# Kernel tuning notes

Measured on AMD Instinct MI355X. Metric: run time of the kernel, lower is better.

## Reference

```python
import jax, jax.numpy as jnp
import numpy as np

N_NODES = 50000
N_EDGES = 800000
D = 128
N_LAYERS = 3
BN_EPS = 1e-5


def setup_inputs() -> dict:
    key = jax.random.key(0)
    ks = jax.random.split(key, 12)
    x = jax.random.normal(ks[0], (N_NODES, D), dtype=jnp.float32)
    edge_index = jax.random.randint(ks[1], (2, N_EDGES), 0, N_NODES, dtype=jnp.int64)
    edge_attr = jnp.zeros((N_EDGES,), dtype=jnp.int32)  # unused by BaseGIN
    edge_weight = jax.random.uniform(ks[2], (N_EDGES,), dtype=jnp.float32)
    s = 1.0 / np.sqrt(D)
    W1 = jax.random.uniform(ks[3], (N_LAYERS, D, D), minval=-s, maxval=s, dtype=jnp.float32)
    b1 = jax.random.uniform(ks[4], (N_LAYERS, D), minval=-s, maxval=s, dtype=jnp.float32)
    W2 = jax.random.uniform(ks[5], (N_LAYERS, D, D), minval=-s, maxval=s, dtype=jnp.float32)
    b2 = jax.random.uniform(ks[6], (N_LAYERS, D), minval=-s, maxval=s, dtype=jnp.float32)
    eps = jnp.zeros((N_LAYERS,), dtype=jnp.float32)          # GIN epsilon, init 0
    gamma = jnp.ones((N_LAYERS, D), dtype=jnp.float32)       # BN weight
    beta = jnp.zeros((N_LAYERS, D), dtype=jnp.float32)       # BN bias
    return {"x": x, "edge_index": edge_index, "edge_attr": edge_attr,
            "edge_weight": edge_weight, "W1": W1, "b1": b1, "W2": W2,
            "b2": b2, "eps": eps, "gamma": gamma, "beta": beta}


def reference(x, edge_index, edge_attr, edge_weight, W1, b1, W2, b2, eps, gamma, beta):
    del edge_attr  # deleted in BaseGIN.forward
    src, dst = edge_index[0], edge_index[1]
    ew = edge_weight[:, None]  # [E, 1], matches edge_weight[:, None] in torch
    n = x.shape[0]
    for i in range(N_LAYERS):
        # GINConv: propagate = scatter-add of gathered x[src] * edge_weight
        msg = x[src] * ew                                   # [E, D]
        agg = jax.ops.segment_sum(msg, dst, num_segments=n)  # [N, D]
        h = (1.0 + eps[i]) * x + agg
        # MLP: Linear -> ReLU -> Linear
        h = jnp.maximum(h @ W1[i] + b1[i], 0.0) @ W2[i] + b2[i]
        # BatchNorm1d (training-mode batch statistics, biased variance)
        mu = jnp.mean(h, axis=0)
        var = jnp.mean((h - mu) ** 2, axis=0)
        h = gamma[i] * (h - mu) * jax.lax.rsqrt(var + BN_EPS) + beta[i]
        h = jnp.maximum(h, 0.0)  # ReLU (dropout p=0.0 -> identity)
        x = x + h  # residual
    return x
```

## Files before the change

kernel.cpp:

```cpp
#include <hip/hip_runtime.h>

#define NN 50000
#define NE 800000
#define DD 128
#define D4 32
#define NBUCK 196
#define CAP 5120
#define BIN_EDGES 8192

typedef __attribute__((ext_vector_type(8))) short short8;
typedef __attribute__((ext_vector_type(4))) float f32x4;

__device__ __forceinline__ unsigned short f2bf(float f) {
    unsigned u = __float_as_uint(f);
    unsigned r = u + 0x7FFF + ((u >> 16) & 1);
    return (unsigned short)(r >> 16);
}
__device__ __forceinline__ float bf2f(unsigned short s) {
    return __uint_as_float(((unsigned)s) << 16);
}


__global__ void x2b(const float4* __restrict__ xin, ushort4* __restrict__ xb) {
    int i = blockIdx.x * blockDim.x + threadIdx.x;
    if (i >= NN * D4) return;
    float4 v = xin[i];
    ushort4 o;
    o.x = f2bf(v.x); o.y = f2bf(v.y); o.z = f2bf(v.z); o.w = f2bf(v.w);
    xb[i] = o;
}


__global__ void prep_wt(const float* __restrict__ W1, const float* __restrict__ W2,
                        unsigned short* __restrict__ Wt) {
    int i = blockIdx.x * blockDim.x + threadIdx.x;
    if (i >= 6 * 16384) return;
    int m = i >> 14;
    int r = i & 16383;
    int n = r >> 7;
    int k = r & 127;
    const float* Ws = (m < 3) ? (W1 + m * 16384) : (W2 + (m - 3) * 16384);
    Wt[i] = f2bf(Ws[k * 128 + n]);
}


__global__ void init_bcur(int* __restrict__ bcur) {
    int t = threadIdx.x;
    if (t < NBUCK) bcur[t] = t * CAP;
}

__global__ void __launch_bounds__(256) bin_pass(const int* __restrict__ ei,
                                                const float* __restrict__ ew,
                                                int* __restrict__ bcur,
                                                int2* __restrict__ staging) {
    __shared__ int cnt[256], off[256], cur[256], gb[256];
    __shared__ int2 bin[BIN_EDGES];
    int tid = threadIdx.x;
    int e0 = blockIdx.x * BIN_EDGES;
    int ne = NE - e0; if (ne > BIN_EDGES) ne = BIN_EDGES;
    cnt[tid] = 0;
    __syncthreads();
    for (int i = tid; i < ne; i += 256) {
        int dst = ei[NE + e0 + i];
        atomicAdd(&cnt[dst >> 8], 1);
    }
    __syncthreads();
    off[tid] = cnt[tid];
    __syncthreads();
    for (int o = 1; o < 256; o <<= 1) {
        int v = off[tid];
        int add = (tid >= o) ? off[tid - o] : 0;
        __syncthreads();
        off[tid] = v + add;
        __syncthreads();
    }
    cur[tid] = off[tid] - cnt[tid];
    __syncthreads();
    for (int i = tid; i < ne; i += 256) {
        int e = e0 + i;
        int dst = ei[NE + e];
        unsigned pack = (((unsigned)ei[e]) << 16) | (unsigned)f2bf(ew[e]);
        int p = atomicAdd(&cur[dst >> 8], 1);
        bin[p] = make_int2((int)pack, dst & 255);
    }
    __syncthreads();
    if (tid < NBUCK) gb[tid] = atomicAdd(&bcur[tid], cnt[tid]);
    __syncthreads();
    for (int i = tid; i < ne; i += 256) {
        int lo = 0, hi = NBUCK - 1;
        while (lo < hi) {
            int mid = (lo + hi) >> 1;
            if (off[mid] > i) hi = mid; else lo = mid + 1;
        }
        int local = i - (off[lo] - cnt[lo]);
        staging[gb[lo] + local] = bin[i];
    }
}

__global__ void scan_buckets(const int* __restrict__ bcur, int* __restrict__ bb2) {
    __shared__ int sh[256];
    int tid = threadIdx.x;
    int c = (tid < NBUCK) ? (bcur[tid] - tid * CAP) : 0;
    sh[tid] = c;
    __syncthreads();
    for (int o = 1; o < 256; o <<= 1) {
        int v = sh[tid];
        int add = (tid >= o) ? sh[tid - o] : 0;
        __syncthreads();
        sh[tid] += 0;
        sh[tid] = v + add;
        __syncthreads();
    }
    if (tid < NBUCK) bb2[tid] = sh[tid] - c;
}

__global__ void __launch_bounds__(256) place_pass(const int2* __restrict__ staging,
                                                  const int* __restrict__ bcur,
                                                  const int* __restrict__ bb2,
                                                  int* __restrict__ rowptr,
                                                  unsigned* __restrict__ srcw) {
    __shared__ int hist[256], off[256], cur[256];
    __shared__ unsigned outb[CAP];
    int b = blockIdx.x;
    int tid = threadIdx.x;
    int sbase = b * CAP;
    int nb = bcur[b] - sbase;
    int bucketBase = bb2[b];
    hist[tid] = 0;
    __syncthreads();
    for (int i = tid; i < nb; i += 256) atomicAdd(&hist[staging[sbase + i].y], 1);
    __syncthreads();
    off[tid] = hist[tid];
    __syncthreads();
    for (int o = 1; o < 256; o <<= 1) {
        int v = off[tid];
        int add = (tid >= o) ? off[tid - o] : 0;
        __syncthreads();
        off[tid] = v + add;
        __syncthreads();
    }
    int excl = off[tid] - hist[tid];
    cur[tid] = excl;
    int node = b * 256 + tid;
    if (node < NN) rowptr[node] = bucketBase + excl;
    if (b == 0 && tid == 0) rowptr[NN] = NE;
    __syncthreads();
    for (int i = tid; i < nb; i += 256) {
        int2 r = staging[sbase + i];
        int p = atomicAdd(&cur[r.y], 1);
        outb[p] = (unsigned)r.x;
    }
    __syncthreads();
    for (int i = tid; i < nb; i += 256) srcw[bucketBase + i] = outb[i];
}


__global__ void __launch_bounds__(256) gather_kernel(
    const unsigned short* __restrict__ xb, const unsigned* __restrict__ srcw,
    const int* __restrict__ rowptr, const float* __restrict__ epsp,
    unsigned short* __restrict__ g, float* __restrict__ stats) {
    if (blockIdx.x == 0) stats[threadIdx.x] = 0.f;
    int node = blockIdx.x * 8 + (threadIdx.x >> 5);
    int lane = threadIdx.x & 31;
    if (node >= NN) return;
    float epsv = 1.0f + *epsp;
    int beg = rowptr[node], end = rowptr[node + 1];
    const ushort4* xb4 = (const ushort4*)xb;
    ushort4 xv = xb4[node * D4 + lane];
    float4 acc = make_float4(bf2f(xv.x) * epsv, bf2f(xv.y) * epsv,
                             bf2f(xv.z) * epsv, bf2f(xv.w) * epsv);
    int i = beg;
    for (; i + 1 < end; i += 2) {
        unsigned sw0 = srcw[i];
        unsigned sw1 = srcw[i + 1];
        ushort4 r0 = xb4[(sw0 >> 16) * D4 + lane];
        ushort4 r1 = xb4[(sw1 >> 16) * D4 + lane];
        float w0 = bf2f((unsigned short)(sw0 & 0xffff));
        float w1 = bf2f((unsigned short)(sw1 & 0xffff));
        acc.x += bf2f(r0.x) * w0; acc.y += bf2f(r0.y) * w0;
        acc.z += bf2f(r0.z) * w0; acc.w += bf2f(r0.w) * w0;
        acc.x += bf2f(r1.x) * w1; acc.y += bf2f(r1.y) * w1;
        acc.z += bf2f(r1.z) * w1; acc.w += bf2f(r1.w) * w1;
    }
    if (i < end) {
        unsigned sw = srcw[i];
        ushort4 r = xb4[(sw >> 16) * D4 + lane];
        float w = bf2f((unsigned short)(sw & 0xffff));
        acc.x += bf2f(r.x) * w; acc.y += bf2f(r.y) * w;
        acc.z += bf2f(r.z) * w; acc.w += bf2f(r.w) * w;
    }
    ushort4 o;
    o.x = f2bf(acc.x); o.y = f2bf(acc.y); o.z = f2bf(acc.z); o.w = f2bf(acc.w);
    ((ushort4*)g)[node * D4 + lane] = o;
}


#define GM 64

template <int MODE>
__global__ void __launch_bounds__(256) mfma_gemm(
    const unsigned short* __restrict__ A,
    const unsigned short* __restrict__ Wt,
    const float* __restrict__ bias,
    unsigned short* __restrict__ outB, float* __restrict__ stats) {
    __shared__ unsigned short As[GM * 128];

    int tid = threadIdx.x;
    int wave = tid >> 6;
    int lane = tid & 63;
    int q = lane >> 4;
    int ml = lane & 15;
    int r0 = blockIdx.x * GM;

#pragma unroll
    for (int i = 0; i < GM / 16; i++) {
        int idx = i * 256 + tid;
        int row = idx >> 4;
        int c = idx & 15;
        float4 v = make_float4(0.f, 0.f, 0.f, 0.f);
        int grow = r0 + row;
        if (grow < NN) v = *(const float4*)(A + grow * DD + c * 8);
        int cs = c ^ (row & 15);
        *(float4*)(&As[row * DD + cs * 8]) = v;
    }

    short8 Bf[2][4];
#pragma unroll
    for (int t = 0; t < 2; t++)
#pragma unroll
        for (int ks = 0; ks < 4; ks++) {
            int n = wave * 32 + t * 16 + ml;
            Bf[t][ks] = *(const short8*)(Wt + n * DD + ks * 32 + q * 8);
        }

    float bvl[2] = {bias[wave * 32 + ml], bias[wave * 32 + 16 + ml]};

    __syncthreads();

    float s[2] = {0.f, 0.f}, s2[2] = {0.f, 0.f};

    for (int rt = 0; rt < GM / 16; rt++) {
        int arow = rt * 16 + ml;
        short8 Af[4];
#pragma unroll
        for (int ks = 0; ks < 4; ks++) {
            int cs = (ks * 4 + q) ^ (arow & 15);
            Af[ks] = *(const short8*)(&As[arow * DD + cs * 8]);
        }
        f32x4 acc[2] = {{0.f, 0.f, 0.f, 0.f}, {0.f, 0.f, 0.f, 0.f}};
#pragma unroll
        for (int ks = 0; ks < 4; ks++) {
            acc[0] = __builtin_amdgcn_mfma_f32_16x16x32_bf16(Af[ks], Bf[0][ks], acc[0], 0, 0, 0);
            acc[1] = __builtin_amdgcn_mfma_f32_16x16x32_bf16(Af[ks], Bf[1][ks], acc[1], 0, 0, 0);
        }
#pragma unroll
        for (int t = 0; t < 2; t++) {
            int col = wave * 32 + t * 16 + ml;
#pragma unroll
            for (int r = 0; r < 4; r++) {
                int grow = r0 + rt * 16 + q * 4 + r;
                if (grow < NN) {
                    float v = acc[t][r] + bvl[t];
                    if (MODE == 0) {
                        outB[grow * DD + col] = f2bf(fmaxf(v, 0.f));
                    } else {
                        outB[grow * DD + col] = f2bf(v);
                        s[t] += v;
                        s2[t] += v * v;
                    }
                }
            }
        }
    }

    if (MODE == 1) {
#pragma unroll
        for (int t = 0; t < 2; t++) {
            float a = s[t], b = s2[t];
            a += __shfl_xor(a, 16); b += __shfl_xor(b, 16);
            a += __shfl_xor(a, 32); b += __shfl_xor(b, 32);
            if (q == 0) {
                int col = wave * 32 + t * 16 + ml;
                atomicAdd(&stats[col], a);
                atomicAdd(&stats[DD + col], b);
            }
        }
    }
}


__global__ void bn_apply(const unsigned short* __restrict__ hb, const float* __restrict__ stats,
                         const float* __restrict__ gamma, const float* __restrict__ beta,
                         const unsigned short* __restrict__ xbin, ushort4* __restrict__ xbout,
                         float4* __restrict__ xf32) {
    int i = blockIdx.x * blockDim.x + threadIdx.x;
    if (i >= NN * D4) return;
    int c4 = i & 31;
    const float invN = 1.0f / NN;
    float4 s = ((const float4*)stats)[c4];
    float4 s2 = ((const float4*)stats)[D4 + c4];
    float4 mu = make_float4(s.x * invN, s.y * invN, s.z * invN, s.w * invN);
    float4 var = make_float4(s2.x * invN - mu.x * mu.x, s2.y * invN - mu.y * mu.y,
                             s2.z * invN - mu.z * mu.z, s2.w * invN - mu.w * mu.w);
    float4 inv = make_float4(rsqrtf(var.x + 1e-5f), rsqrtf(var.y + 1e-5f),
                             rsqrtf(var.z + 1e-5f), rsqrtf(var.w + 1e-5f));
    float4 g = ((const float4*)gamma)[c4];
    float4 b = ((const float4*)beta)[c4];
    ushort4 hu = ((const ushort4*)hb)[i];
    float4 hv = make_float4(bf2f(hu.x), bf2f(hu.y), bf2f(hu.z), bf2f(hu.w));
    ushort4 xu = ((const ushort4*)xbin)[i];
    float4 xv = make_float4(bf2f(xu.x), bf2f(xu.y), bf2f(xu.z), bf2f(xu.w));
    float4 v = make_float4(fmaxf(g.x * (hv.x - mu.x) * inv.x + b.x, 0.f),
                           fmaxf(g.y * (hv.y - mu.y) * inv.y + b.y, 0.f),
                           fmaxf(g.z * (hv.z - mu.z) * inv.z + b.z, 0.f),
                           fmaxf(g.w * (hv.w - mu.w) * inv.w + b.w, 0.f));
    float4 o = make_float4(xv.x + v.x, xv.y + v.y, xv.z + v.z, xv.w + v.w);
    if (xbout) {
        ushort4 ob;
        ob.x = f2bf(o.x); ob.y = f2bf(o.y); ob.z = f2bf(o.z); ob.w = f2bf(o.w);
        xbout[i] = ob;
    }
    if (xf32) xf32[i] = o;
}


extern "C" void kernel_launch(void* const* d_in, const int* in_sizes, int n_in,
                              void* d_out, int out_size, void* d_ws, size_t ws_size,
                              hipStream_t stream) {
    const float* x_in = (const float*)d_in[0];
    const int* ei = (const int*)d_in[1];
    const float* ew = (const float*)d_in[3];
    const float* W1 = (const float*)d_in[4];
    const float* b1 = (const float*)d_in[5];
    const float* W2 = (const float*)d_in[6];
    const float* b2 = (const float*)d_in[7];
    const float* eps = (const float*)d_in[8];
    const float* gamma = (const float*)d_in[9];
    const float* beta = (const float*)d_in[10];

    float* x = (float*)d_out;

    char* ws = (char*)d_ws;
    unsigned short* g = (unsigned short*)ws;
    unsigned short* t = (unsigned short*)(ws + 12800000);
    unsigned short* hb = (unsigned short*)(ws + 25600000);
    int2* staging = (int2*)(ws + 25600000);
    unsigned short* xb = (unsigned short*)(ws + 38400000);
    float* stats = (float*)(ws + 51200000);
    int* rowptr = (int*)(ws + 51201024);
    unsigned short* Wtall = (unsigned short*)(ws + 51401216);
    unsigned* srcw = (unsigned*)(ws + 51597824);
    int* bcur = (int*)(ws + 54797824);
    int* bb2 = (int*)(ws + 54798848);

    const int n4x = NN * D4;

    init_bcur<<<1, 256, 0, stream>>>(bcur);
    bin_pass<<<(NE + BIN_EDGES - 1) / BIN_EDGES, 256, 0, stream>>>(ei, ew, bcur, staging);
    scan_buckets<<<1, 256, 0, stream>>>(bcur, bb2);
    place_pass<<<NBUCK, 256, 0, stream>>>(staging, bcur, bb2, rowptr, srcw);

    prep_wt<<<(6 * 16384 + 255) / 256, 256, 0, stream>>>(W1, W2, Wtall);

    x2b<<<(n4x + 255) / 256, 256, 0, stream>>>((const float4*)x_in, (ushort4*)xb);

    const int gemmGrid = (NN + GM - 1) / GM;

    for (int i = 0; i < 3; i++) {
        const float* b1i = b1 + i * DD;
        const float* b2i = b2 + i * DD;
        const unsigned short* Wt1 = Wtall + i * 16384;
        const unsigned short* Wt2 = Wtall + (3 + i) * 16384;

        gather_kernel<<<(NN + 7) / 8, 256, 0, stream>>>(xb, srcw, rowptr, eps + i, g, stats);

        mfma_gemm<0><<<gemmGrid, 256, 0, stream>>>(g, Wt1, b1i, t, nullptr);

        mfma_gemm<1><<<gemmGrid, 256, 0, stream>>>(t, Wt2, b2i, hb, stats);

        bn_apply<<<(n4x + 255) / 256, 256, 0, stream>>>(
            hb, stats, gamma + i * DD, beta + i * DD, xb,
            (i < 2) ? (ushort4*)xb : nullptr,
            (i == 2) ? (float4*)x : nullptr);
    }
}
```

Baseline: 412.7 us.

## Simplify edge binning: register-held edges, smaller blocks, no LDS sort

```diff
diff --git a/kernel.cpp b/kernel.cpp
--- a/kernel.cpp
+++ b/kernel.cpp
@@ -6,7 +6,7 @@
 #define D4 32
 #define NBUCK 196
 #define CAP 5120
-#define BIN_EDGES 8192
+#define BIN_EDGES 2048
 
 typedef __attribute__((ext_vector_type(8))) short short8;
 typedef __attribute__((ext_vector_type(4))) float f32x4;
@@ -53,47 +53,38 @@
                                                 const float* __restrict__ ew,
                                                 int* __restrict__ bcur,
                                                 int2* __restrict__ staging) {
-    __shared__ int cnt[256], off[256], cur[256], gb[256];
-    __shared__ int2 bin[BIN_EDGES];
+    __shared__ int cnt[256], base[256], cur[256];
     int tid = threadIdx.x;
     int e0 = blockIdx.x * BIN_EDGES;
     int ne = NE - e0; if (ne > BIN_EDGES) ne = BIN_EDGES;
     cnt[tid] = 0;
-    __syncthreads();
-    for (int i = tid; i < ne; i += 256) {
-        int dst = ei[NE + e0 + i];
-        atomicAdd(&cnt[dst >> 8], 1);
-    }
-    __syncthreads();
-    off[tid] = cnt[tid];
-    __syncthreads();
-    for (int o = 1; o < 256; o <<= 1) {
-        int v = off[tid];
-        int add = (tid >= o) ? off[tid - o] : 0;
-        __syncthreads();
-        off[tid] = v + add;
-        __syncthreads();
-    }
-    cur[tid] = off[tid] - cnt[tid];
-    __syncthreads();
-    for (int i = tid; i < ne; i += 256) {
-        int e = e0 + i;
-        int dst = ei[NE + e];
-        unsigned pack = (((unsigned)ei[e]) << 16) | (unsigned)f2bf(ew[e]);
-        int p = atomicAdd(&cur[dst >> 8], 1);
-        bin[p] = make_int2((int)pack, dst & 255);
-    }
-    __syncthreads();
-    if (tid < NBUCK) gb[tid] = atomicAdd(&bcur[tid], cnt[tid]);
-    __syncthreads();
-    for (int i = tid; i < ne; i += 256) {
-        int lo = 0, hi = NBUCK - 1;
-        while (lo < hi) {
-            int mid = (lo + hi) >> 1;
-            if (off[mid] > i) hi = mid; else lo = mid + 1;
-        }
-        int local = i - (off[lo] - cnt[lo]);
-        staging[gb[lo] + local] = bin[i];
+    cur[tid] = 0;
+    __syncthreads();
+    int dstv[BIN_EDGES / 256];
+    unsigned packv[BIN_EDGES / 256];
+#pragma unroll
+    for (int j = 0; j < BIN_EDGES / 256; j++) {
+        int i = j * 256 + tid;
+        dstv[j] = -1;
+        if (i < ne) {
+            int e = e0 + i;
+            int dst = ei[NE + e];
+            dstv[j] = dst;
+            packv[j] = (((unsigned)ei[e]) << 16) | (unsigned)f2bf(ew[e]);
+            atomicAdd(&cnt[dst >> 8], 1);
+        }
+    }
+    __syncthreads();
+    if (tid < NBUCK && cnt[tid] > 0) base[tid] = atomicAdd(&bcur[tid], cnt[tid]);
+    __syncthreads();
+#pragma unroll
+    for (int j = 0; j < BIN_EDGES / 256; j++) {
+        int dst = dstv[j];
+        if (dst >= 0) {
+            int b = dst >> 8;
+            int p = atomicAdd(&cur[b], 1);
+            staging[base[b] + p] = make_int2((int)packv[j], dst & 255);
+        }
     }
 }
 
@@ -107,7 +98,6 @@
         int v = sh[tid];
         int add = (tid >= o) ? sh[tid - o] : 0;
         __syncthreads();
-        sh[tid] += 0;
         sh[tid] = v + add;
         __syncthreads();
     }
```

New measurement: 387.9 us. -6.0%, faster.
